# Kernel tuning notes

Measured on AMD Instinct MI355X. Metric: run time of the kernel, lower is better.

Reference implementation:

```python
import jax, jax.numpy as jnp
import numpy as np

N = 30000
E = 600000
IN = 64
HID = 128
EPS = 1e-5
HEADS_PER_LAYER = (4, 4, 1)


def _bn(x, g, b):
    # eval-mode BatchNorm: running_mean=0, running_var=1
    return x * (g / np.sqrt(1.0 + EPS)) + b


def _segment_softmax(e, dst, n):
    m = jax.ops.segment_max(e, dst, num_segments=n)
    ex = jnp.exp(e - m[dst])
    s = jax.ops.segment_sum(ex, dst, num_segments=n)
    return ex / (s[dst] + 1e-16)


def _gcn_conv(x, w, b, src, dst, norm, n):
    m = (x @ w)[src] * norm[:, None]            # [E+N, HID]
    return jax.ops.segment_sum(m, dst, num_segments=n) + b


def _gat_conv(x, w, a_src, a_dst, b, src, dst, n, heads):
    C = HID // heads
    xh = (x @ w).reshape(n, heads, C)
    asrc = (xh * a_src.reshape(heads, C)).sum(-1)   # [N, heads]
    adst = (xh * a_dst.reshape(heads, C)).sum(-1)
    e = jax.nn.leaky_relu(asrc[src] + adst[dst], 0.2)  # [E+N, heads]
    alpha = _segment_softmax(e, dst, n)
    out = jax.ops.segment_sum(xh[src] * alpha[:, :, None], dst, num_segments=n)
    return out.reshape(n, HID) + b


def _forward(x, gcn_in_w, gcn_in_b, gcn_res_w, gcn_res_b, gcn_w, gcn_b,
             gcn_bn_g, gcn_bn_b, gcn_c1w, gcn_c1b, gcn_c2w, gcn_c2b,
             gcn_c3w, gcn_c3b, gat_in_w, gat_in_b, gat_w, gat_asrc,
             gat_adst, gat_b, gat_bn_g, gat_bn_b, feat_imp, gat_c1w,
             gat_c1b, gat_cbn_g, gat_cbn_b, gat_c2w, gat_c2b, gat_c3w,
             gat_c3b, fin_w, fin_b, fin_bn_g, fin_bn_b, fin2_w, fin2_b,
             edge_index):
    n = x.shape[0]
    loop = jnp.arange(n, dtype=edge_index.dtype)
    src = jnp.concatenate([edge_index[0], loop])  # add self-loops
    dst = jnp.concatenate([edge_index[1], loop])
    # GCN symmetric normalization (with self-loops)
    deg = jax.ops.segment_sum(jnp.ones_like(dst, dtype=x.dtype), dst, num_segments=n)
    dis = jnp.where(deg > 0, jax.lax.rsqrt(jnp.maximum(deg, 1.0)), 0.0)
    norm = dis[src] * dis[dst]

    # ---- GCN branch (eval: dropout = identity, self-attn skipped since N>5000) ----
    xp = x @ gcn_in_w + gcn_in_b
    res = x @ gcn_res_w + gcn_res_b
    for i in range(3):
        xn = _gcn_conv(xp, gcn_w[i], gcn_b[i], src, dst, norm, n)
        xn = jax.nn.relu(_bn(xn, gcn_bn_g[i], gcn_bn_b[i]))
        if i % 2 == 1:
            xp = xn + res
            res = xp
        else:
            xp = xn
    h = jax.nn.relu(xp @ gcn_c1w + gcn_c1b)
    h = jax.nn.relu(h @ gcn_c2w + gcn_c2b)
    gcn_out = h @ gcn_c3w + gcn_c3b

    # ---- GAT branch ----
    xg = x @ gat_in_w + gat_in_b
    for i in range(3):
        xg = _gat_conv(xg, gat_w[i], gat_asrc[i], gat_adst[i], gat_b[i],
                       src, dst, n, HEADS_PER_LAYER[i])
        xg = jax.nn.elu(_bn(xg, gat_bn_g[i], gat_bn_b[i]))
    xg = xg * feat_imp
    h = jax.nn.relu(xg @ gat_c1w + gat_c1b)
    h = _bn(h, gat_cbn_g, gat_cbn_b)
    h = jax.nn.relu(h @ gat_c2w + gat_c2b)
    gat_out = h @ gat_c3w + gat_c3b

    # ---- fusion: N > 10000 -> weighted blend path ----
    fused = 0.6 * gcn_out + 0.4 * gat_out
    h = jax.nn.relu(fused @ fin_w + fin_b)
    h = _bn(h, fin_bn_g, fin_bn_b)
    return h @ fin2_w + fin2_b  # [N, 2]


def setup_inputs() -> dict:
    key = jax.random.key(0)
    ks = iter(jax.random.split(key, 64))

    def nrm(shape, scale=1.0):
        return jax.random.normal(next(ks), shape, dtype=jnp.float32) * scale

    s_in = 1.0 / np.sqrt(IN)
    s_h = 1.0 / np.sqrt(HID)
    inp = {}
    inp['x'] = nrm((N, IN))
    inp['edge_index'] = jax.random.randint(next(ks), (2, E), 0, N, dtype=jnp.int32)
    inp['gcn_in_w'] = nrm((IN, HID), s_in); inp['gcn_in_b'] = nrm((HID,), 0.01)
    inp['gcn_res_w'] = nrm((IN, HID), s_in); inp['gcn_res_b'] = nrm((HID,), 0.01)
    inp['gcn_w'] = nrm((3, HID, HID), s_h); inp['gcn_b'] = nrm((3, HID), 0.01)
    inp['gcn_bn_g'] = 1.0 + nrm((3, HID), 0.1); inp['gcn_bn_b'] = nrm((3, HID), 0.1)
    inp['gcn_c1w'] = nrm((HID, 64), s_h); inp['gcn_c1b'] = nrm((64,), 0.01)
    inp['gcn_c2w'] = nrm((64, 32), 0.125); inp['gcn_c2b'] = nrm((32,), 0.01)
    inp['gcn_c3w'] = nrm((32, HID), 0.18); inp['gcn_c3b'] = nrm((HID,), 0.01)
    inp['gat_in_w'] = nrm((IN, HID), s_in); inp['gat_in_b'] = nrm((HID,), 0.01)
    inp['gat_w'] = nrm((3, HID, HID), s_h)
    inp['gat_asrc'] = nrm((3, HID), s_h); inp['gat_adst'] = nrm((3, HID), s_h)
    inp['gat_b'] = nrm((3, HID), 0.01)
    inp['gat_bn_g'] = 1.0 + nrm((3, HID), 0.1); inp['gat_bn_b'] = nrm((3, HID), 0.1)
    inp['feat_imp'] = 1.0 + nrm((HID,), 0.1)
    inp['gat_c1w'] = nrm((HID, 64), s_h); inp['gat_c1b'] = nrm((64,), 0.01)
    inp['gat_cbn_g'] = 1.0 + nrm((64,), 0.1); inp['gat_cbn_b'] = nrm((64,), 0.1)
    inp['gat_c2w'] = nrm((64, 32), 0.125); inp['gat_c2b'] = nrm((32,), 0.01)
    inp['gat_c3w'] = nrm((32, HID), 0.18); inp['gat_c3b'] = nrm((HID,), 0.01)
    inp['fin_w'] = nrm((HID, 64), s_h); inp['fin_b'] = nrm((64,), 0.01)
    inp['fin_bn_g'] = 1.0 + nrm((64,), 0.1); inp['fin_bn_b'] = nrm((64,), 0.1)
    inp['fin2_w'] = nrm((64, 2), 0.125); inp['fin2_b'] = nrm((2,), 0.01)
    return inp


def reference(x, edge_index, gcn_in_w, gcn_in_b, gcn_res_w, gcn_res_b, gcn_w,
              gcn_b, gcn_bn_g, gcn_bn_b, gcn_c1w, gcn_c1b, gcn_c2w, gcn_c2b,
              gcn_c3w, gcn_c3b, gat_in_w, gat_in_b, gat_w, gat_asrc, gat_adst,
              gat_b, gat_bn_g, gat_bn_b, feat_imp, gat_c1w, gat_c1b, gat_cbn_g,
              gat_cbn_b, gat_c2w, gat_c2b, gat_c3w, gat_c3b, fin_w, fin_b,
              fin_bn_g, fin_bn_b, fin2_w, fin2_b):
    return _forward(x, gcn_in_w, gcn_in_b, gcn_res_w, gcn_res_b, gcn_w, gcn_b,
                    gcn_bn_g, gcn_bn_b, gcn_c1w, gcn_c1b, gcn_c2w, gcn_c2b,
                    gcn_c3w, gcn_c3b, gat_in_w, gat_in_b, gat_w, gat_asrc,
                    gat_adst, gat_b, gat_bn_g, gat_bn_b, feat_imp, gat_c1w,
                    gat_c1b, gat_cbn_g, gat_cbn_b, gat_c2w, gat_c2b, gat_c3w,
                    gat_c3b, fin_w, fin_b, fin_bn_g, fin_bn_b, fin2_w, fin2_b,
                    edge_index)
```

## Files before the change

### kernel.cpp

```cpp
#include <hip/hip_runtime.h>
#include <hip/hip_fp16.h>

#define RSQ_BN 0.9999950000374997f

typedef _Float16 f16x8 __attribute__((ext_vector_type(8)));
typedef float f32x4 __attribute__((ext_vector_type(4)));

union H8u { uint4 u4; __half h[8]; };

__device__ __forceinline__ float leaky02(float x) { return x > 0.f ? x : 0.2f * x; }

__device__ __forceinline__ float4 ld4(const float* p) {
    return *reinterpret_cast<const float4*>(p);
}
__device__ __forceinline__ void st4(float* p, float4 v) {
    *reinterpret_cast<float4*>(p) = v;
}
__device__ __forceinline__ void ld8(float* d, const float* p) {
    float4 u = ld4(p), v = ld4(p + 4);
    d[0] = u.x; d[1] = u.y; d[2] = u.z; d[3] = u.w;
    d[4] = v.x; d[5] = v.y; d[6] = v.z; d[7] = v.w;
}
__device__ __forceinline__ void st8(float* p, const float* v) {
    st4(p, make_float4(v[0], v[1], v[2], v[3]));
    st4(p + 4, make_float4(v[4], v[5], v[6], v[7]));
}


__global__ void hist_k(const int* __restrict__ edst, int* __restrict__ cnt, int E, int EN) {
    int i = blockIdx.x * 256 + threadIdx.x;
    if (i >= EN) return;
    int d = (i < E) ? edst[i] : (i - E);
    atomicAdd(&cnt[d], 1);
}

__global__ __launch_bounds__(256)
void scanA_k(const int* __restrict__ cnt, int* __restrict__ rowptr,
             int* __restrict__ bsum, int n) {
    __shared__ int sh[256];
    int t = threadIdx.x;
    int i = blockIdx.x * 256 + t;
    int v = (i < n) ? cnt[i] : 0;
    sh[t] = v;
    __syncthreads();
#pragma unroll
    for (int off = 1; off < 256; off <<= 1) {
        int u = 0;
        if (t >= off) u = sh[t - off];
        __syncthreads();
        sh[t] += u;
        __syncthreads();
    }
    if (i < n) rowptr[i] = sh[t] - v;
    if (t == 255) bsum[blockIdx.x] = sh[255];
}

__global__ __launch_bounds__(256)
void scanB_k(int* __restrict__ bsum, int nb) {
    __shared__ int sh[256];
    int t = threadIdx.x;
    int v = (t < nb) ? bsum[t] : 0;
    sh[t] = v;
    __syncthreads();
#pragma unroll
    for (int off = 1; off < 256; off <<= 1) {
        int u = 0;
        if (t >= off) u = sh[t - off];
        __syncthreads();
        sh[t] += u;
        __syncthreads();
    }
    if (t < nb) bsum[t] = sh[t] - v;
}

__global__ __launch_bounds__(256)
void scanC_k(const int* __restrict__ cnt, const int* __restrict__ bsum,
             int* __restrict__ rowptr, int* __restrict__ cursor,
             float* __restrict__ dis, int n, int EN) {
    int i = blockIdx.x * 256 + threadIdx.x;
    if (i < n) {
        int r = rowptr[i] + bsum[blockIdx.x];
        rowptr[i] = r;
        cursor[i] = r;
        dis[i] = rsqrtf((float)cnt[i]);
    }
    if (i == 0) rowptr[n] = EN;
}

__global__ void scatter_k(const int* __restrict__ esrc, const int* __restrict__ edst,
                          int* __restrict__ cursor, int* __restrict__ colidx, int E, int EN) {
    int i = blockIdx.x * 256 + threadIdx.x;
    if (i >= EN) return;
    int s, d;
    if (i < E) { s = esrc[i]; d = edst[i]; }
    else       { s = i - E; d = s; }
    int pos = atomicAdd(&cursor[d], 1);
    colidx[pos] = s;
}


__global__ void wtx_all_k(const float* __restrict__ gcn_in_w, const float* __restrict__ gcn_res_w,
                          const float* __restrict__ gat_in_w,
                          const float* __restrict__ gcn_w, const float* __restrict__ gat_w,
                          const float* __restrict__ gcn_c1w, const float* __restrict__ gat_c1w,
                          const float* __restrict__ gcn_c3w, const float* __restrict__ gat_c3w,
                          const float* __restrict__ fin_w,
                          const float* __restrict__ gcn_c2w, const float* __restrict__ gat_c2w,
                          const float* __restrict__ gat_asrc, const float* __restrict__ gat_adst,
                          __half* __restrict__ WTin, __half* __restrict__ WTg,
                          __half* __restrict__ WTa, __half* __restrict__ WTc1,
                          __half* __restrict__ WTc3, __half* __restrict__ WTfin,
                          __half* __restrict__ WTc2, __half* __restrict__ WTd) {
    int idx = blockIdx.x * 256 + threadIdx.x;
    const float* src;
    __half* dst;
    int K, M, o;
    if (idx < 24576) {
        int mi = idx >> 13; o = idx & 8191;
        src = mi == 0 ? gcn_in_w : (mi == 1 ? gcn_res_w : gat_in_w);
        dst = WTin + mi * 8192; K = 64; M = 128;
    } else if (idx < 73728) {
        int r = idx - 24576; int mi = r >> 14; o = r & 16383;
        src = gcn_w + mi * 16384; dst = WTg + mi * 16384; K = 128; M = 128;
    } else if (idx < 122880) {
        int r = idx - 73728; int mi = r >> 14; o = r & 16383;
        src = gat_w + mi * 16384; dst = WTa + mi * 16384; K = 128; M = 128;
    } else if (idx < 139264) {
        int r = idx - 122880; int mi = r >> 13; o = r & 8191;
        src = mi ? gat_c1w : gcn_c1w; dst = WTc1 + mi * 8192; K = 128; M = 64;
    } else if (idx < 147456) {
        int r = idx - 139264; int mi = r >> 12; o = r & 4095;
        src = mi ? gat_c3w : gcn_c3w; dst = WTc3 + mi * 4096; K = 32; M = 128;
    } else if (idx < 155648) {
        o = idx - 147456; src = fin_w; dst = WTfin; K = 128; M = 64;
    } else if (idx < 159744) {
        int r = idx - 155648; int mi = r >> 11; o = r & 2047;
        src = mi ? gat_c2w : gcn_c2w; dst = WTc2 + mi * 2048; K = 64; M = 32;
    } else if (idx < 165888) {
        int r = idx - 159744;
        int layer = r >> 11; o = r & 2047;
        int col = o >> 7, k = o & 127;
        int hh = (layer < 2) ? 4 : 1;
        int C = 128 / hh;
        float v = 0.f;
        if (col < hh) {
            const float* w = gat_w + (size_t)(layer * 128 + k) * 128 + col * C;
            const float* av = gat_asrc + layer * 128 + col * C;
            for (int c2 = 0; c2 < C; ++c2) v += w[c2] * av[c2];
        } else if (col >= 8 && col < 8 + hh) {
            int hthis = col - 8;
            const float* w = gat_w + (size_t)(layer * 128 + k) * 128 + hthis * C;
            const float* av = gat_adst + layer * 128 + hthis * C;
            for (int c2 = 0; c2 < C; ++c2) v += w[c2] * av[c2];
        }
        WTd[(size_t)layer * 2048 + o] = (__half)v;
        return;
    } else return;
    int mcol = o / K, k = o - mcol * K;
    dst[o] = (__half)src[k * M + mcol];
}


__device__ __forceinline__ f16x8 mk_af(const float* xr, int kb) {
    float4 v0 = ld4(xr + kb), v1 = ld4(xr + kb + 4);
    f16x8 af;
    af[0] = (_Float16)v0.x; af[1] = (_Float16)v0.y;
    af[2] = (_Float16)v0.z; af[3] = (_Float16)v0.w;
    af[4] = (_Float16)v1.x; af[5] = (_Float16)v1.y;
    af[6] = (_Float16)v1.z; af[7] = (_Float16)v1.w;
    return af;
}

__global__ __launch_bounds__(256)
void mfma_lin3_k(const float* __restrict__ X, const __half* __restrict__ WTin,
                 const float* __restrict__ b0, float* __restrict__ Y0,
                 const float* __restrict__ b1, float* __restrict__ Y1,
                 const float* __restrict__ b2, float* __restrict__ Y2,
                 int n, int gper) {
    constexpr int K = 64, CT = 8;
    int set = blockIdx.x / gper, blk = blockIdx.x % gper;
    const __half* WT = WTin + (size_t)set * 8192;
    const float* bi = set == 0 ? b0 : (set == 1 ? b1 : b2);
    float* Y = set == 0 ? Y0 : (set == 1 ? Y1 : Y2);
    int wave = threadIdx.x >> 6, lane = threadIdx.x & 63;
    int m = lane & 15, quad = lane >> 4;
    int row0 = blk * 64 + wave * 16;
    int arow = min(row0 + m, n - 1);
    const float* xr = X + (size_t)arow * K;
    f32x4 acc[CT];
#pragma unroll
    for (int ct = 0; ct < CT; ++ct) acc[ct] = (f32x4){0.f, 0.f, 0.f, 0.f};
#pragma unroll
    for (int k32 = 0; k32 < K / 32; ++k32) {
        int kb = k32 * 32 + quad * 8;
        f16x8 af = mk_af(xr, kb);
#pragma unroll
        for (int ct = 0; ct < CT; ++ct) {
            f16x8 bf = *reinterpret_cast<const f16x8*>(WT + (size_t)(ct * 16 + m) * K + kb);
            acc[ct] = __builtin_amdgcn_mfma_f32_16x16x32_f16(af, bf, acc[ct], 0, 0, 0);
        }
    }
#pragma unroll
    for (int ct = 0; ct < CT; ++ct) {
        int col = ct * 16 + m;
        float cb = bi[col];
#pragma unroll
        for (int reg = 0; reg < 4; ++reg) {
            int row = row0 + quad * 4 + reg;
            if (row < n) Y[(size_t)row * 128 + col] = acc[ct][reg] + cb;
        }
    }
}


__global__ __launch_bounds__(256)
void dual128_mfma_k(const float* __restrict__ Xg, const __half* __restrict__ WTg,
                    __half* __restrict__ Yg,
                    const float* __restrict__ Xa, const __half* __restrict__ WTa,
                    __half* __restrict__ Ya,
                    const float* __restrict__ dis,
                    const __half* __restrict__ WTd,
                    float* __restrict__ avp, float* __restrict__ bvp,
                    int hh, int n, int gper) {
    bool gat = blockIdx.x >= gper;
    int blk = gat ? blockIdx.x - gper : blockIdx.x;
    const float* X = gat ? Xa : Xg;
    const __half* WT = gat ? WTa : WTg;
    __half* Y = gat ? Ya : Yg;
    int wave = threadIdx.x >> 6;
    int lane = threadIdx.x & 63;
    int m = lane & 15, quad = lane >> 4;
    int row0 = blk * 64 + wave * 16;
    int arow = min(row0 + m, n - 1);
    const float* xr = X + (size_t)arow * 128;
    f32x4 acc[8];
#pragma unroll
    for (int ct = 0; ct < 8; ++ct) acc[ct] = (f32x4){0.f, 0.f, 0.f, 0.f};
    if (!gat) {
#pragma unroll
        for (int k32 = 0; k32 < 4; ++k32) {
            int kb = k32 * 32 + quad * 8;
            f16x8 af = mk_af(xr, kb);
#pragma unroll
            for (int ct = 0; ct < 8; ++ct) {
                f16x8 bf = *reinterpret_cast<const f16x8*>(WT + (size_t)(ct * 16 + m) * 128 + kb);
                acc[ct] = __builtin_amdgcn_mfma_f32_16x16x32_f16(af, bf, acc[ct], 0, 0, 0);
            }
        }
#pragma unroll
        for (int reg = 0; reg < 4; ++reg) {
            int row = row0 + quad * 4 + reg;
            if (row < n) {
                float dv = dis[row];
#pragma unroll
                for (int ct = 0; ct < 8; ++ct)
                    Y[(size_t)row * 128 + ct * 16 + m] = (__half)(acc[ct][reg] * dv);
            }
        }
    } else {
        f32x4 accd = (f32x4){0.f, 0.f, 0.f, 0.f};
#pragma unroll
        for (int k32 = 0; k32 < 4; ++k32) {
            int kb = k32 * 32 + quad * 8;
            f16x8 af = mk_af(xr, kb);
#pragma unroll
            for (int ct = 0; ct < 8; ++ct) {
                f16x8 bf = *reinterpret_cast<const f16x8*>(WT + (size_t)(ct * 16 + m) * 128 + kb);
                acc[ct] = __builtin_amdgcn_mfma_f32_16x16x32_f16(af, bf, acc[ct], 0, 0, 0);
            }
            f16x8 bd = *reinterpret_cast<const f16x8*>(WTd + (size_t)m * 128 + kb);
            accd = __builtin_amdgcn_mfma_f32_16x16x32_f16(af, bd, accd, 0, 0, 0);
        }
#pragma unroll
        for (int reg = 0; reg < 4; ++reg) {
            int row = row0 + quad * 4 + reg;
            if (row < n) {
#pragma unroll
                for (int ct = 0; ct < 8; ++ct)
                    Y[(size_t)row * 128 + ct * 16 + m] = (__half)acc[ct][reg];
                if (m < hh) avp[row * hh + m] = accd[reg];
                else if (m >= 8 && m < 8 + hh) bvp[row * hh + (m - 8)] = accd[reg];
            }
        }
    }
}


__global__ __launch_bounds__(256)
void fused_gather_k(const int* __restrict__ rowptr, const int* __restrict__ colidx,
                    const float* __restrict__ dis,
                    const __half* __restrict__ Tg, const float* __restrict__ gbias,
                    const float* __restrict__ gbng, const float* __restrict__ gbnb,
                    const float* __restrict__ res, float* __restrict__ Yg,
                    const __half* __restrict__ Ta, const float* __restrict__ avp,
                    const float* __restrict__ bvp, const float* __restrict__ abias,
                    const float* __restrict__ abng, const float* __restrict__ abnb,
                    const float* __restrict__ fimp, float* __restrict__ Ya,
                    int n, int hh, int log2C) {
    int idx = blockIdx.x * 256 + threadIdx.x;
    int i = idx >> 5;
    if (i >= n) return;
    int half = (idx >> 4) & 1;
    int c = (idx & 15) * 8;
    int h = c >> log2C;
    float ad = bvp[i * hh + h];
    int q0 = rowptr[i], q1 = rowptr[i + 1];
    int cnt0 = (q1 - q0 + 1) >> 1;
    int p0 = half ? q0 + cnt0 : q0;
    int p1 = half ? q1 : q0 + cnt0;
    float g[8], a[8];
#pragma unroll
    for (int t = 0; t < 8; ++t) { g[t] = 0.f; a[t] = 0.f; }
    float m = -3.0e38f, s = 0.f;

    int deg = p1 - p0;
    int ng = (deg + 3) >> 2;
    int p = p0;
    int sx[4]; float av[4], vm[4];
    if (ng > 0) {
#pragma unroll
        for (int j = 0; j < 4; ++j) {
            int q = p + j;
            vm[j] = (q < p1) ? 1.f : 0.f;
            sx[j] = colidx[min(q, p1 - 1)];
        }
#pragma unroll
        for (int j = 0; j < 4; ++j) av[j] = avp[sx[j] * hh + h];
    }
    for (int gi = 0; gi < ng; ++gi) {
        uint4 qg[4], qa[4];
#pragma unroll
        for (int j = 0; j < 4; ++j)
            qg[j] = *reinterpret_cast<const uint4*>(Tg + (size_t)sx[j] * 128 + c);
#pragma unroll
        for (int j = 0; j < 4; ++j)
            qa[j] = *reinterpret_cast<const uint4*>(Ta + (size_t)sx[j] * 128 + c);
        int pn = p + 4;
        int sn[4]; float avn[4], vmn[4];
#pragma unroll
        for (int j = 0; j < 4; ++j) {
            int q = pn + j;
            vmn[j] = (q < p1) ? 1.f : 0.f;
            sn[j] = colidx[min(max(q, p0), p1 - 1)];
        }
#pragma unroll
        for (int j = 0; j < 4; ++j) avn[j] = avp[sn[j] * hh + h];
        float e0 = vm[0] > 0.f ? leaky02(av[0] + ad) : -3.0e38f;
        float e1 = vm[1] > 0.f ? leaky02(av[1] + ad) : -3.0e38f;
        float e2 = vm[2] > 0.f ? leaky02(av[2] + ad) : -3.0e38f;
        float e3 = vm[3] > 0.f ? leaky02(av[3] + ad) : -3.0e38f;
        float mc = fmaxf(fmaxf(e0, e1), fmaxf(e2, e3));
        float mn = fmaxf(m, mc);
        float scale = __expf(m - mn);
        float w0 = __expf(e0 - mn), w1 = __expf(e1 - mn);
        float w2 = __expf(e2 - mn), w3 = __expf(e3 - mn);
        s = s * scale + (w0 + w1 + w2 + w3);
        m = mn;
        {
            H8u k0, k1, k2, k3;
            k0.u4 = qg[0]; k1.u4 = qg[1]; k2.u4 = qg[2]; k3.u4 = qg[3];
#pragma unroll
            for (int t = 0; t < 8; ++t) {
                float v = g[t];
                v = fmaf(__half2float(k0.h[t]), vm[0], v);
                v = fmaf(__half2float(k1.h[t]), vm[1], v);
                v = fmaf(__half2float(k2.h[t]), vm[2], v);
                v = fmaf(__half2float(k3.h[t]), vm[3], v);
                g[t] = v;
            }
        }
        {
            H8u k0, k1, k2, k3;
            k0.u4 = qa[0]; k1.u4 = qa[1]; k2.u4 = qa[2]; k3.u4 = qa[3];
#pragma unroll
            for (int t = 0; t < 8; ++t) {
                float v = a[t] * scale;
                v = fmaf(__half2float(k0.h[t]), w0, v);
                v = fmaf(__half2float(k1.h[t]), w1, v);
                v = fmaf(__half2float(k2.h[t]), w2, v);
                v = fmaf(__half2float(k3.h[t]), w3, v);
                a[t] = v;
            }
        }
        p = pn;
#pragma unroll
        for (int j = 0; j < 4; ++j) { sx[j] = sn[j]; av[j] = avn[j]; vm[j] = vmn[j]; }
    }

    {
        float m2 = __shfl_xor(m, 16);
        float s2 = __shfl_xor(s, 16);
        float mn = fmaxf(m, m2);
        float wA = __expf(m - mn), wB = __expf(m2 - mn);
        s = s * wA + s2 * wB;
#pragma unroll
        for (int t = 0; t < 8; ++t) {
            float g2 = __shfl_xor(g[t], 16);
            float a2 = __shfl_xor(a[t], 16);
            g[t] += g2;
            a[t] = a[t] * wA + a2 * wB;
        }
    }
    if (half) return;

    {
        float di = dis[i];
        float bb[8], gg[8], nb[8];
        ld8(bb, gbias + c); ld8(gg, gbng + c); ld8(nb, gbnb + c);
        float o[8];
#pragma unroll
        for (int t = 0; t < 8; ++t) {
            float v = g[t] * di + bb[t];
            o[t] = fmaxf(v * (gg[t] * RSQ_BN) + nb[t], 0.f);
        }
        if (res) {
            float rr[8]; ld8(rr, res + (size_t)i * 128 + c);
#pragma unroll
            for (int t = 0; t < 8; ++t) o[t] += rr[t];
        }
        st8(Yg + (size_t)i * 128 + c, o);
    }
    {
        float si = 1.f / (s + 1e-16f);
        float bb[8], gg[8], nb[8];
        ld8(bb, abias + c); ld8(gg, abng + c); ld8(nb, abnb + c);
        float o[8];
#pragma unroll
        for (int t = 0; t < 8; ++t) {
            float v = a[t] * si + bb[t];
            v = v * (gg[t] * RSQ_BN) + nb[t];
            o[t] = v > 0.f ? v : expm1f(v);
        }
        if (fimp) {
            float ff[8]; ld8(ff, fimp + c);
#pragma unroll
            for (int t = 0; t < 8; ++t) o[t] *= ff[t];
        }
        st8(Ya + (size_t)i * 128 + c, o);
    }
}


__global__ __launch_bounds__(256)
void fused_tail_k(const float* __restrict__ Xg, const float* __restrict__ Xa,
                  const __half* __restrict__ WTc1,
                  const float* __restrict__ c1bg, const float* __restrict__ c1ba,
                  const float* __restrict__ cbng, const float* __restrict__ cbnb,
                  const __half* __restrict__ WTc2,
                  const float* __restrict__ c2bg, const float* __restrict__ c2ba,
                  const __half* __restrict__ WTc3,
                  const float* __restrict__ c3bg, const float* __restrict__ c3ba,
                  const __half* __restrict__ WTfin, const float* __restrict__ finb,
                  const float* __restrict__ fbng, const float* __restrict__ fbnb,
                  const float* __restrict__ w2, const float* __restrict__ b2,
                  float* __restrict__ out, int n) {
    __shared__ alignas(16) __half h1s[2][64][88];
    __shared__ alignas(16) __half h2s[2][64][56];
    __shared__ alignas(16) __half Fs[64][152];
    int wave = threadIdx.x >> 6, lane = threadIdx.x & 63;
    int m = lane & 15, quad = lane >> 4;
    int row0 = blockIdx.x * 64 + wave * 16;
    int lr0 = wave * 16;
    int arow = min(row0 + m, n - 1);

#pragma unroll
    for (int br = 0; br < 2; ++br) {
        const float* xr = (br ? Xa : Xg) + (size_t)arow * 128;
        const __half* WT = WTc1 + br * 8192;
        f32x4 acc[4];
#pragma unroll
        for (int ct = 0; ct < 4; ++ct) acc[ct] = (f32x4){0.f, 0.f, 0.f, 0.f};
#pragma unroll
        for (int k32 = 0; k32 < 4; ++k32) {
            int kb = k32 * 32 + quad * 8;
            f16x8 af = mk_af(xr, kb);
#pragma unroll
            for (int ct = 0; ct < 4; ++ct) {
                f16x8 bf = *reinterpret_cast<const f16x8*>(WT + (ct * 16 + m) * 128 + kb);
                acc[ct] = __builtin_amdgcn_mfma_f32_16x16x32_f16(af, bf, acc[ct], 0, 0, 0);
            }
        }
        const float* bi = br ? c1ba : c1bg;
#pragma unroll
        for (int ct = 0; ct < 4; ++ct) {
            int col = ct * 16 + m;
            float cb = bi[col];
            float cg = br ? cbng[col] * RSQ_BN : 1.f;
            float cbb = br ? cbnb[col] : 0.f;
#pragma unroll
            for (int reg = 0; reg < 4; ++reg) {
                float v = fmaxf(acc[ct][reg] + cb, 0.f) * cg + cbb;
                h1s[br][lr0 + quad * 4 + reg][col] = (__half)v;
            }
        }
    }
    __syncthreads();
#pragma unroll
    for (int br = 0; br < 2; ++br) {
        f32x4 acc[2];
        acc[0] = (f32x4){0.f, 0.f, 0.f, 0.f};
        acc[1] = (f32x4){0.f, 0.f, 0.f, 0.f};
        const __half* WT = WTc2 + br * 2048;
#pragma unroll
        for (int k32 = 0; k32 < 2; ++k32) {
            int kb = k32 * 32 + quad * 8;
            f16x8 af = *reinterpret_cast<const f16x8*>(&h1s[br][lr0 + m][kb]);
#pragma unroll
            for (int ct = 0; ct < 2; ++ct) {
                f16x8 bf = *reinterpret_cast<const f16x8*>(WT + (ct * 16 + m) * 64 + kb);
                acc[ct] = __builtin_amdgcn_mfma_f32_16x16x32_f16(af, bf, acc[ct], 0, 0, 0);
            }
        }
        const float* bi = br ? c2ba : c2bg;
#pragma unroll
        for (int ct = 0; ct < 2; ++ct) {
            int col = ct * 16 + m;
            float cb = bi[col];
#pragma unroll
            for (int reg = 0; reg < 4; ++reg) {
                float v = fmaxf(acc[ct][reg] + cb, 0.f);
                h2s[br][lr0 + quad * 4 + reg][col] = (__half)v;
            }
        }
    }
    __syncthreads();
    {
        f32x4 ag[8], aa[8];
#pragma unroll
        for (int ct = 0; ct < 8; ++ct) {
            ag[ct] = (f32x4){0.f, 0.f, 0.f, 0.f};
            aa[ct] = (f32x4){0.f, 0.f, 0.f, 0.f};
        }
        int kb = quad * 8;
        f16x8 afg = *reinterpret_cast<const f16x8*>(&h2s[0][lr0 + m][kb]);
        f16x8 afa = *reinterpret_cast<const f16x8*>(&h2s[1][lr0 + m][kb]);
#pragma unroll
        for (int ct = 0; ct < 8; ++ct) {
            f16x8 bfg = *reinterpret_cast<const f16x8*>(WTc3 + (ct * 16 + m) * 32 + kb);
            f16x8 bfa = *reinterpret_cast<const f16x8*>(WTc3 + 4096 + (ct * 16 + m) * 32 + kb);
            ag[ct] = __builtin_amdgcn_mfma_f32_16x16x32_f16(afg, bfg, ag[ct], 0, 0, 0);
            aa[ct] = __builtin_amdgcn_mfma_f32_16x16x32_f16(afa, bfa, aa[ct], 0, 0, 0);
        }
#pragma unroll
        for (int ct = 0; ct < 8; ++ct) {
            int col = ct * 16 + m;
            float cb = 0.6f * c3bg[col] + 0.4f * c3ba[col];
#pragma unroll
            for (int reg = 0; reg < 4; ++reg) {
                float v = 0.6f * ag[ct][reg] + 0.4f * aa[ct][reg] + cb;
                Fs[lr0 + quad * 4 + reg][col] = (__half)v;
            }
        }
    }
    __syncthreads();
    {
        f32x4 acc[4];
#pragma unroll
        for (int ct = 0; ct < 4; ++ct) acc[ct] = (f32x4){0.f, 0.f, 0.f, 0.f};
#pragma unroll
        for (int k32 = 0; k32 < 4; ++k32) {
            int kb = k32 * 32 + quad * 8;
            f16x8 af = *reinterpret_cast<const f16x8*>(&Fs[lr0 + m][kb]);
#pragma unroll
            for (int ct = 0; ct < 4; ++ct) {
                f16x8 bf = *reinterpret_cast<const f16x8*>(WTfin + (ct * 16 + m) * 128 + kb);
                acc[ct] = __builtin_amdgcn_mfma_f32_16x16x32_f16(af, bf, acc[ct], 0, 0, 0);
            }
        }
        float p0[4] = {0.f, 0.f, 0.f, 0.f}, p1[4] = {0.f, 0.f, 0.f, 0.f};
#pragma unroll
        for (int ct = 0; ct < 4; ++ct) {
            int col = ct * 16 + m;
            float cb = finb[col];
            float cg = fbng[col] * RSQ_BN;
            float cbb = fbnb[col];
            float w20 = w2[2 * col], w21 = w2[2 * col + 1];
#pragma unroll
            for (int reg = 0; reg < 4; ++reg) {
                float v = fmaxf(acc[ct][reg] + cb, 0.f) * cg + cbb;
                p0[reg] += v * w20;
                p1[reg] += v * w21;
            }
        }
        for (int off = 1; off < 16; off <<= 1) {
#pragma unroll
            for (int reg = 0; reg < 4; ++reg) {
                p0[reg] += __shfl_xor(p0[reg], off);
                p1[reg] += __shfl_xor(p1[reg], off);
            }
        }
        if (m == 0) {
#pragma unroll
            for (int reg = 0; reg < 4; ++reg) {
                int row = row0 + quad * 4 + reg;
                if (row < n) {
                    out[row * 2] = p0[reg] + b2[0];
                    out[row * 2 + 1] = p1[reg] + b2[1];
                }
            }
        }
    }
}


static inline int cdiv(int a, int b) { return (a + b - 1) / b; }

extern "C" void kernel_launch(void* const* d_in, const int* in_sizes, int n_in,
                              void* d_out, int out_size, void* d_ws, size_t ws_size,
                              hipStream_t stream) {
    const float* x       = (const float*)d_in[0];
    const int*   ei      = (const int*)d_in[1];
    const float* gcn_in_w = (const float*)d_in[2];
    const float* gcn_in_b = (const float*)d_in[3];
    const float* gcn_res_w = (const float*)d_in[4];
    const float* gcn_res_b = (const float*)d_in[5];
    const float* gcn_w   = (const float*)d_in[6];
    const float* gcn_b   = (const float*)d_in[7];
    const float* gcn_bn_g = (const float*)d_in[8];
    const float* gcn_bn_b = (const float*)d_in[9];
    const float* gcn_c1w = (const float*)d_in[10];
    const float* gcn_c1b = (const float*)d_in[11];
    const float* gcn_c2w = (const float*)d_in[12];
    const float* gcn_c2b = (const float*)d_in[13];
    const float* gcn_c3w = (const float*)d_in[14];
    const float* gcn_c3b = (const float*)d_in[15];
    const float* gat_in_w = (const float*)d_in[16];
    const float* gat_in_b = (const float*)d_in[17];
    const float* gat_w   = (const float*)d_in[18];
    const float* gat_asrc = (const float*)d_in[19];
    const float* gat_adst = (const float*)d_in[20];
    const float* gat_b   = (const float*)d_in[21];
    const float* gat_bn_g = (const float*)d_in[22];
    const float* gat_bn_b = (const float*)d_in[23];
    const float* feat_imp = (const float*)d_in[24];
    const float* gat_c1w = (const float*)d_in[25];
    const float* gat_c1b = (const float*)d_in[26];
    const float* gat_cbn_g = (const float*)d_in[27];
    const float* gat_cbn_b = (const float*)d_in[28];
    const float* gat_c2w = (const float*)d_in[29];
    const float* gat_c2b = (const float*)d_in[30];
    const float* gat_c3w = (const float*)d_in[31];
    const float* gat_c3b = (const float*)d_in[32];
    const float* fin_w   = (const float*)d_in[33];
    const float* fin_b   = (const float*)d_in[34];
    const float* fin_bn_g = (const float*)d_in[35];
    const float* fin_bn_b = (const float*)d_in[36];
    const float* fin2_w  = (const float*)d_in[37];
    const float* fin2_b  = (const float*)d_in[38];

    const int N = in_sizes[0] / 64;
    const int E = in_sizes[1] / 2;
    const int EN = E + N;
    const int* esrc = ei;
    const int* edst = ei + E;

    char* wp = (char*)d_ws;
    auto alloc = [&](size_t bytes) -> void* {
        void* p = (void*)wp;
        wp += (bytes + 255) & ~(size_t)255;
        return p;
    };
    int* cnt    = (int*)alloc((size_t)N * 4);
    int* rowptr = (int*)alloc((size_t)(N + 1) * 4);
    int* cursor = (int*)alloc((size_t)N * 4);
    int* bsum   = (int*)alloc((size_t)256 * 4);
    int* colidx = (int*)alloc((size_t)EN * 4);
    float* dis  = (float*)alloc((size_t)N * 4);
    float* A    = (float*)alloc((size_t)N * 128 * 4);
    float* B    = (float*)alloc((size_t)N * 128 * 4);
    float* G    = (float*)alloc((size_t)N * 128 * 4);
    float* H    = (float*)alloc((size_t)N * 128 * 4);
    float* R    = (float*)alloc((size_t)N * 128 * 4);
    __half* Th1 = (__half*)alloc((size_t)N * 128 * 2);
    __half* Th2 = (__half*)alloc((size_t)N * 128 * 2);
    float* avv  = (float*)alloc((size_t)N * 4 * 4);
    float* bvv  = (float*)alloc((size_t)N * 4 * 4);
    __half* WTin = (__half*)alloc((size_t)3 * 8192 * 2);
    __half* WTg  = (__half*)alloc((size_t)3 * 16384 * 2);
    __half* WTa  = (__half*)alloc((size_t)3 * 16384 * 2);
    __half* WTc1 = (__half*)alloc((size_t)2 * 8192 * 2);
    __half* WTc3 = (__half*)alloc((size_t)2 * 4096 * 2);
    __half* WTfin = (__half*)alloc((size_t)8192 * 2);
    __half* WTc2 = (__half*)alloc((size_t)2 * 2048 * 2);
    __half* WTd  = (__half*)alloc((size_t)3 * 2048 * 2);

    const int nScanB = cdiv(N, 256);
    hipMemsetAsync(cnt, 0, (size_t)N * 4, stream);
    hist_k<<<cdiv(EN, 256), 256, 0, stream>>>(edst, cnt, E, EN);
    scanA_k<<<nScanB, 256, 0, stream>>>(cnt, rowptr, bsum, N);
    scanB_k<<<1, 256, 0, stream>>>(bsum, nScanB);
    scanC_k<<<nScanB, 256, 0, stream>>>(cnt, bsum, rowptr, cursor, dis, N, EN);
    scatter_k<<<cdiv(EN, 256), 256, 0, stream>>>(esrc, edst, cursor, colidx, E, EN);
    wtx_all_k<<<648, 256, 0, stream>>>(gcn_in_w, gcn_res_w, gat_in_w, gcn_w, gat_w,
                                       gcn_c1w, gat_c1w, gcn_c3w, gat_c3w, fin_w,
                                       gcn_c2w, gat_c2w, gat_asrc, gat_adst,
                                       WTin, WTg, WTa, WTc1, WTc3, WTfin, WTc2, WTd);

    const int g64r = cdiv(N, 64);
    const int gG   = cdiv(N, 8);

    mfma_lin3_k<<<3 * g64r, 256, 0, stream>>>(x, WTin, gcn_in_b, A, gcn_res_b, R,
                                              gat_in_b, G, N, g64r);

    const int heads_arr[3] = {4, 4, 1};
    float* gcur = A; float* gnxt = B;
    float* acur = G; float* anxt = H;
    for (int i = 0; i < 3; ++i) {
        int hh = heads_arr[i];
        int log2C = (hh == 4) ? 5 : 7;
        dual128_mfma_k<<<2 * g64r, 256, 0, stream>>>(gcur, WTg + (size_t)i * 16384, Th1,
                                                     acur, WTa + (size_t)i * 16384, Th2, dis,
                                                     WTd + (size_t)i * 2048,
                                                     avv, bvv, hh, N, g64r);
        fused_gather_k<<<gG, 256, 0, stream>>>(rowptr, colidx, dis,
                                               Th1, gcn_b + i * 128, gcn_bn_g + i * 128,
                                               gcn_bn_b + i * 128, (i == 1) ? R : nullptr, gnxt,
                                               Th2, avv, bvv, gat_b + i * 128,
                                               gat_bn_g + i * 128, gat_bn_b + i * 128,
                                               (i == 2) ? feat_imp : nullptr, anxt,
                                               N, hh, log2C);
        float* t = gcur; gcur = gnxt; gnxt = t;
        t = acur; acur = anxt; anxt = t;
    }

    fused_tail_k<<<g64r, 256, 0, stream>>>(gcur, acur,
                                           WTc1, gcn_c1b, gat_c1b, gat_cbn_g, gat_cbn_b,
                                           WTc2, gcn_c2b, gat_c2b,
                                           WTc3, gcn_c3b, gat_c3b,
                                           WTfin, fin_b, fin_bn_g, fin_bn_b,
                                           fin2_w, fin2_b, (float*)d_out, N);
}
```

Baseline: 485.6 us.

## Store intermediate activations in fp16 and restructure gather to split tables per thread

Intermediate node-feature buffers (A, B, G, H, R) change from fp32 to fp16. Downstream MFMA kernels now load their A operands directly as f16x8 instead of converting from float, which halves activation memory traffic. The gather kernel is remapped so each group of 4 threads handles one node and a 16-column slice, with separate threads walking the GCN table and the GAT table over the full edge list. This drops the cross-half shuffle reduction, and colidx is read with nontemporal loads. The cost is lower precision in the intermediates and redundant softmax bookkeeping on the GCN-table threads.

After: 849.4 us. 74.9% more time.

```diff
diff --git a/kernel.cpp b/kernel.cpp
--- a/kernel.cpp
+++ b/kernel.cpp
@@ -20,10 +20,6 @@
     float4 u = ld4(p), v = ld4(p + 4);
     d[0] = u.x; d[1] = u.y; d[2] = u.z; d[3] = u.w;
     d[4] = v.x; d[5] = v.y; d[6] = v.z; d[7] = v.w;
-}
-__device__ __forceinline__ void st8(float* p, const float* v) {
-    st4(p, make_float4(v[0], v[1], v[2], v[3]));
-    st4(p + 4, make_float4(v[4], v[5], v[6], v[7]));
 }
 
 
@@ -173,15 +169,15 @@
 
 __global__ __launch_bounds__(256)
 void mfma_lin3_k(const float* __restrict__ X, const __half* __restrict__ WTin,
-                 const float* __restrict__ b0, float* __restrict__ Y0,
-                 const float* __restrict__ b1, float* __restrict__ Y1,
-                 const float* __restrict__ b2, float* __restrict__ Y2,
+                 const float* __restrict__ b0, __half* __restrict__ Y0,
+                 const float* __restrict__ b1, __half* __restrict__ Y1,
+                 const float* __restrict__ b2, __half* __restrict__ Y2,
                  int n, int gper) {
     constexpr int K = 64, CT = 8;
     int set = blockIdx.x / gper, blk = blockIdx.x % gper;
     const __half* WT = WTin + (size_t)set * 8192;
     const float* bi = set == 0 ? b0 : (set == 1 ? b1 : b2);
-    float* Y = set == 0 ? Y0 : (set == 1 ? Y1 : Y2);
+    __half* Y = set == 0 ? Y0 : (set == 1 ? Y1 : Y2);
     int wave = threadIdx.x >> 6, lane = threadIdx.x & 63;
     int m = lane & 15, quad = lane >> 4;
     int row0 = blk * 64 + wave * 16;
@@ -207,16 +203,16 @@
 #pragma unroll
         for (int reg = 0; reg < 4; ++reg) {
             int row = row0 + quad * 4 + reg;
-            if (row < n) Y[(size_t)row * 128 + col] = acc[ct][reg] + cb;
+            if (row < n) Y[(size_t)row * 128 + col] = (__half)(acc[ct][reg] + cb);
         }
     }
 }
 
 
 __global__ __launch_bounds__(256)
-void dual128_mfma_k(const float* __restrict__ Xg, const __half* __restrict__ WTg,
+void dual128_mfma_k(const __half* __restrict__ Xg, const __half* __restrict__ WTg,
                     __half* __restrict__ Yg,
-                    const float* __restrict__ Xa, const __half* __restrict__ WTa,
+                    const __half* __restrict__ Xa, const __half* __restrict__ WTa,
                     __half* __restrict__ Ya,
                     const float* __restrict__ dis,
                     const __half* __restrict__ WTd,
@@ -224,7 +220,7 @@
                     int hh, int n, int gper) {
     bool gat = blockIdx.x >= gper;
     int blk = gat ? blockIdx.x - gper : blockIdx.x;
-    const float* X = gat ? Xa : Xg;
+    const __half* X = gat ? Xa : Xg;
     const __half* WT = gat ? WTa : WTg;
     __half* Y = gat ? Ya : Yg;
     int wave = threadIdx.x >> 6;
@@ -232,7 +228,7 @@
     int m = lane & 15, quad = lane >> 4;
     int row0 = blk * 64 + wave * 16;
     int arow = min(row0 + m, n - 1);
-    const float* xr = X + (size_t)arow * 128;
+    const __half* xr = X + (size_t)arow * 128;
     f32x4 acc[8];
 #pragma unroll
     for (int ct = 0; ct < 8; ++ct) acc[ct] = (f32x4){0.f, 0.f, 0.f, 0.f};
@@ -240,7 +236,7 @@
 #pragma unroll
         for (int k32 = 0; k32 < 4; ++k32) {
             int kb = k32 * 32 + quad * 8;
-            f16x8 af = mk_af(xr, kb);
+            f16x8 af = *reinterpret_cast<const f16x8*>(xr + kb);
 #pragma unroll
             for (int ct = 0; ct < 8; ++ct) {
                 f16x8 bf = *reinterpret_cast<const f16x8*>(WT + (size_t)(ct * 16 + m) * 128 + kb);
@@ -262,7 +258,7 @@
 #pragma unroll
         for (int k32 = 0; k32 < 4; ++k32) {
             int kb = k32 * 32 + quad * 8;
-            f16x8 af = mk_af(xr, kb);
+            f16x8 af = *reinterpret_cast<const f16x8*>(xr + kb);
 #pragma unroll
             for (int ct = 0; ct < 8; ++ct) {
                 f16x8 bf = *reinterpret_cast<const f16x8*>(WT + (size_t)(ct * 16 + m) * 128 + kb);
@@ -291,57 +287,51 @@
                     const float* __restrict__ dis,
                     const __half* __restrict__ Tg, const float* __restrict__ gbias,
                     const float* __restrict__ gbng, const float* __restrict__ gbnb,
-                    const float* __restrict__ res, float* __restrict__ Yg,
+                    const __half* __restrict__ res, __half* __restrict__ Yg,
                     const __half* __restrict__ Ta, const float* __restrict__ avp,
                     const float* __restrict__ bvp, const float* __restrict__ abias,
                     const float* __restrict__ abng, const float* __restrict__ abnb,
-                    const float* __restrict__ fimp, float* __restrict__ Ya,
+                    const float* __restrict__ fimp, __half* __restrict__ Ya,
                     int n, int hh, int log2C) {
-    int idx = blockIdx.x * 256 + threadIdx.x;
-    int i = idx >> 5;
+    int slice = blockIdx.x & 7;
+    int i = (blockIdx.x >> 3) * 64 + (threadIdx.x >> 2);
     if (i >= n) return;
-    int half = (idx >> 4) & 1;
-    int c = (idx & 15) * 8;
+    int r = threadIdx.x & 3;
+    int tbl = r >> 1;
+    int c = slice * 16 + (r & 1) * 8;
     int h = c >> log2C;
+    const __half* T = tbl ? Ta : Tg;
     float ad = bvp[i * hh + h];
-    int q0 = rowptr[i], q1 = rowptr[i + 1];
-    int cnt0 = (q1 - q0 + 1) >> 1;
-    int p0 = half ? q0 + cnt0 : q0;
-    int p1 = half ? q1 : q0 + cnt0;
-    float g[8], a[8];
-#pragma unroll
-    for (int t = 0; t < 8; ++t) { g[t] = 0.f; a[t] = 0.f; }
+    int p0 = rowptr[i], p1 = rowptr[i + 1];
+    float acc[8];
+#pragma unroll
+    for (int t = 0; t < 8; ++t) acc[t] = 0.f;
     float m = -3.0e38f, s = 0.f;
 
-    int deg = p1 - p0;
-    int ng = (deg + 3) >> 2;
+    int ng = (p1 - p0 + 3) >> 2;
     int p = p0;
     int sx[4]; float av[4], vm[4];
-    if (ng > 0) {
-#pragma unroll
-        for (int j = 0; j < 4; ++j) {
-            int q = p + j;
-            vm[j] = (q < p1) ? 1.f : 0.f;
-            sx[j] = colidx[min(q, p1 - 1)];
-        }
-#pragma unroll
-        for (int j = 0; j < 4; ++j) av[j] = avp[sx[j] * hh + h];
-    }
+#pragma unroll
+    for (int j = 0; j < 4; ++j) {
+        int q = p0 + j;
+        vm[j] = (q < p1) ? 1.f : 0.f;
+        sx[j] = __builtin_nontemporal_load(colidx + min(q, p1 - 1));
+    }
+#pragma unroll
+    for (int j = 0; j < 4; ++j) av[j] = avp[sx[j] * hh + h];
+
     for (int gi = 0; gi < ng; ++gi) {
-        uint4 qg[4], qa[4];
+        uint4 q4[4];
 #pragma unroll
         for (int j = 0; j < 4; ++j)
-            qg[j] = *reinterpret_cast<const uint4*>(Tg + (size_t)sx[j] * 128 + c);
-#pragma unroll
-        for (int j = 0; j < 4; ++j)
-            qa[j] = *reinterpret_cast<const uint4*>(Ta + (size_t)sx[j] * 128 + c);
+            q4[j] = *reinterpret_cast<const uint4*>(T + (size_t)sx[j] * 128 + c);
         int pn = p + 4;
         int sn[4]; float avn[4], vmn[4];
 #pragma unroll
         for (int j = 0; j < 4; ++j) {
             int q = pn + j;
             vmn[j] = (q < p1) ? 1.f : 0.f;
-            sn[j] = colidx[min(max(q, p0), p1 - 1)];
+            sn[j] = __builtin_nontemporal_load(colidx + min(max(q, p0), p1 - 1));
         }
 #pragma unroll
         for (int j = 0; j < 4; ++j) avn[j] = avp[sn[j] * hh + h];
@@ -356,78 +346,55 @@
         float w2 = __expf(e2 - mn), w3 = __expf(e3 - mn);
         s = s * scale + (w0 + w1 + w2 + w3);
         m = mn;
-        {
-            H8u k0, k1, k2, k3;
-            k0.u4 = qg[0]; k1.u4 = qg[1]; k2.u4 = qg[2]; k3.u4 = qg[3];
-#pragma unroll
-            for (int t = 0; t < 8; ++t) {
-                float v = g[t];
-                v = fmaf(__half2float(k0.h[t]), vm[0], v);
-                v = fmaf(__half2float(k1.h[t]), vm[1], v);
-                v = fmaf(__half2float(k2.h[t]), vm[2], v);
-                v = fmaf(__half2float(k3.h[t]), vm[3], v);
-                g[t] = v;
-            }
-        }
-        {
-            H8u k0, k1, k2, k3;
-            k0.u4 = qa[0]; k1.u4 = qa[1]; k2.u4 = qa[2]; k3.u4 = qa[3];
-#pragma unroll
-            for (int t = 0; t < 8; ++t) {
-                float v = a[t] * scale;
-                v = fmaf(__half2float(k0.h[t]), w0, v);
-                v = fmaf(__half2float(k1.h[t]), w1, v);
-                v = fmaf(__half2float(k2.h[t]), w2, v);
-                v = fmaf(__half2float(k3.h[t]), w3, v);
-                a[t] = v;
-            }
+        float u0 = tbl ? w0 : vm[0];
+        float u1 = tbl ? w1 : vm[1];
+        float u2 = tbl ? w2 : vm[2];
+        float u3 = tbl ? w3 : vm[3];
+        float sc = tbl ? scale : 1.f;
+        H8u k0, k1, k2, k3;
+        k0.u4 = q4[0]; k1.u4 = q4[1]; k2.u4 = q4[2]; k3.u4 = q4[3];
+#pragma unroll
+        for (int t = 0; t < 8; ++t) {
+            float v = acc[t] * sc;
+            v = fmaf(__half2float(k0.h[t]), u0, v);
+            v = fmaf(__half2float(k1.h[t]), u1, v);
+            v = fmaf(__half2float(k2.h[t]), u2, v);
+            v = fmaf(__half2float(k3.h[t]), u3, v);
+            acc[t] = v;
         }
         p = pn;
 #pragma unroll
         for (int j = 0; j < 4; ++j) { sx[j] = sn[j]; av[j] = avn[j]; vm[j] = vmn[j]; }
     }
 
-    {
-        float m2 = __shfl_xor(m, 16);
-        float s2 = __shfl_xor(s, 16);
-        float mn = fmaxf(m, m2);
-        float wA = __expf(m - mn), wB = __expf(m2 - mn);
-        s = s * wA + s2 * wB;
-#pragma unroll
-        for (int t = 0; t < 8; ++t) {
-            float g2 = __shfl_xor(g[t], 16);
-            float a2 = __shfl_xor(a[t], 16);
-            g[t] += g2;
-            a[t] = a[t] * wA + a2 * wB;
-        }
-    }
-    if (half) return;
-
-    {
+    if (tbl == 0) {
         float di = dis[i];
         float bb[8], gg[8], nb[8];
         ld8(bb, gbias + c); ld8(gg, gbng + c); ld8(nb, gbnb + c);
         float o[8];
 #pragma unroll
         for (int t = 0; t < 8; ++t) {
-            float v = g[t] * di + bb[t];
+            float v = acc[t] * di + bb[t];
             o[t] = fmaxf(v * (gg[t] * RSQ_BN) + nb[t], 0.f);
         }
         if (res) {
-            float rr[8]; ld8(rr, res + (size_t)i * 128 + c);
-#pragma unroll
-            for (int t = 0; t < 8; ++t) o[t] += rr[t];
-        }
-        st8(Yg + (size_t)i * 128 + c, o);
-    }
-    {
+            H8u rr;
+            rr.u4 = *reinterpret_cast<const uint4*>(res + (size_t)i * 128 + c);
+#pragma unroll
+            for (int t = 0; t < 8; ++t) o[t] += __half2float(rr.h[t]);
+        }
+        H8u w;
+#pragma unroll
+        for (int t = 0; t < 8; ++t) w.h[t] = (__half)o[t];
+        *reinterpret_cast<uint4*>(Yg + (size_t)i * 128 + c) = w.u4;
+    } else {
         float si = 1.f / (s + 1e-16f);
         float bb[8], gg[8], nb[8];
         ld8(bb, abias + c); ld8(gg, abng + c); ld8(nb, abnb + c);
         float o[8];
 #pragma unroll
         for (int t = 0; t < 8; ++t) {
-            float v = a[t] * si + bb[t];
+            float v = acc[t] * si + bb[t];
             v = v * (gg[t] * RSQ_BN) + nb[t];
             o[t] = v > 0.f ? v : expm1f(v);
         }
@@ -436,13 +403,16 @@
 #pragma unroll
             for (int t = 0; t < 8; ++t) o[t] *= ff[t];
         }
-        st8(Ya + (size_t)i * 128 + c, o);
+        H8u w;
+#pragma unroll
+        for (int t = 0; t < 8; ++t) w.h[t] = (__half)o[t];
+        *reinterpret_cast<uint4*>(Ya + (size_t)i * 128 + c) = w.u4;
     }
 }
 
 
 __global__ __launch_bounds__(256)
-void fused_tail_k(const float* __restrict__ Xg, const float* __restrict__ Xa,
+void fused_tail_k(const __half* __restrict__ Xg, const __half* __restrict__ Xa,
                   const __half* __restrict__ WTc1,
                   const float* __restrict__ c1bg, const float* __restrict__ c1ba,
                   const float* __restrict__ cbng, const float* __restrict__ cbnb,
@@ -465,7 +435,7 @@
 
 #pragma unroll
     for (int br = 0; br < 2; ++br) {
-        const float* xr = (br ? Xa : Xg) + (size_t)arow * 128;
+        const __half* xr = (br ? Xa : Xg) + (size_t)arow * 128;
         const __half* WT = WTc1 + br * 8192;
         f32x4 acc[4];
 #pragma unroll
@@ -473,7 +443,7 @@
 #pragma unroll
         for (int k32 = 0; k32 < 4; ++k32) {
             int kb = k32 * 32 + quad * 8;
-            f16x8 af = mk_af(xr, kb);
+            f16x8 af = *reinterpret_cast<const f16x8*>(xr + kb);
 #pragma unroll
             for (int ct = 0; ct < 4; ++ct) {
                 f16x8 bf = *reinterpret_cast<const f16x8*>(WT + (ct * 16 + m) * 128 + kb);
@@ -666,11 +636,11 @@
     int* bsum   = (int*)alloc((size_t)256 * 4);
     int* colidx = (int*)alloc((size_t)EN * 4);
     float* dis  = (float*)alloc((size_t)N * 4);
-    float* A    = (float*)alloc((size_t)N * 128 * 4);
-    float* B    = (float*)alloc((size_t)N * 128 * 4);
-    float* G    = (float*)alloc((size_t)N * 128 * 4);
-    float* H    = (float*)alloc((size_t)N * 128 * 4);
-    float* R    = (float*)alloc((size_t)N * 128 * 4);
+    __half* A   = (__half*)alloc((size_t)N * 128 * 2);
+    __half* B   = (__half*)alloc((size_t)N * 128 * 2);
+    __half* G   = (__half*)alloc((size_t)N * 128 * 2);
+    __half* H   = (__half*)alloc((size_t)N * 128 * 2);
+    __half* R   = (__half*)alloc((size_t)N * 128 * 2);
     __half* Th1 = (__half*)alloc((size_t)N * 128 * 2);
     __half* Th2 = (__half*)alloc((size_t)N * 128 * 2);
     float* avv  = (float*)alloc((size_t)N * 4 * 4);
@@ -697,14 +667,14 @@
                                        WTin, WTg, WTa, WTc1, WTc3, WTfin, WTc2, WTd);
 
     const int g64r = cdiv(N, 64);
-    const int gG   = cdiv(N, 8);
+    const int gG   = 8 * cdiv(N, 64);
 
     mfma_lin3_k<<<3 * g64r, 256, 0, stream>>>(x, WTin, gcn_in_b, A, gcn_res_b, R,
                                               gat_in_b, G, N, g64r);
 
     const int heads_arr[3] = {4, 4, 1};
-    float* gcur = A; float* gnxt = B;
-    float* acur = G; float* anxt = H;
+    __half* gcur = A; __half* gnxt = B;
+    __half* acur = G; __half* anxt = H;
     for (int i = 0; i < 3; ++i) {
         int hh = heads_arr[i];
         int log2C = (hh == 4) ? 5 : 7;
@@ -719,7 +689,7 @@
                                                gat_bn_g + i * 128, gat_bn_b + i * 128,
                                                (i == 2) ? feat_imp : nullptr, anxt,
                                                N, hh, log2C);
-        float* t = gcur; gcur = gnxt; gnxt = t;
+        __half* t = gcur; gcur = gnxt; gnxt = t;
         t = acur; acur = anxt; anxt = t;
     }
 
```
